# Optimization experiments

Hardware: AMD Instinct MI355X
Metric: run time of the kernel (lower is better)

Reference implementation:

```python
import jax, jax.numpy as jnp
import numpy as np

EPS = 1e-5


def spmm(rows, cols, vals, x):
    # x: (B, C, V); y[b,c,v] = sum_{e: rows[e]==v} vals[e] * x[b,c,cols[e]]
    B, C, V = x.shape
    xt = x.reshape(B * C, V).T                      # (V, B*C)
    msg = vals[:, None] * xt[cols]                  # (E, B*C)
    y = jax.ops.segment_sum(msg, rows, num_segments=V)
    return y.T.reshape(B, C, V)


def cheb_conv(x, W, b, rows, cols, vals):
    # W: (K, Cin, Cout); Chebyshev recurrence over node dim
    K = W.shape[0]
    Tk = [x]
    if K > 1:
        Tk.append(spmm(rows, cols, vals, x))
    for _ in range(2, K):
        Tk.append(2.0 * spmm(rows, cols, vals, Tk[-1]) - Tk[-2])
    T = jnp.stack(Tk)                               # (K, B, Cin, V)
    out = jnp.einsum('kbiv,kio->bov', T, W)
    if b is not None:
        out = out + b[None, :, None]
    return out


def bn(x, g, be):
    # BatchNorm1d training-mode stats over (batch, nodes) per channel
    m = jnp.mean(x, axis=(0, 2), keepdims=True)
    v = jnp.var(x, axis=(0, 2), keepdims=True)
    return (x - m) * jax.lax.rsqrt(v + EPS) * g[None, :, None] + be[None, :, None]


def res_block(x, rows, cols, vals, ga, bea, Wa, ba, gb, beb, Wb, bb, Ws=None):
    xn = bn(x, ga, bea)
    out = cheb_conv(xn, Wa, ba, rows, cols, vals)
    out = bn(jax.nn.relu(out), gb, beb)
    out = cheb_conv(out, Wb, bb, rows, cols, vals)
    sc = xn if Ws is None else cheb_conv(xn, Ws, None, rows, cols, vals)
    return jax.nn.relu(out + sc)


def setup_inputs() -> dict:
    key = jax.random.key(0)
    ks = iter(jax.random.split(key, 40))
    V, E, B, K = 50000, 800000, 8, 4
    d = {}
    d['x'] = jax.random.normal(next(ks), (B, 16, V), dtype=jnp.float32)
    d['lap_rows'] = jax.random.randint(next(ks), (E,), 0, V, dtype=jnp.int32)
    d['lap_cols'] = jax.random.randint(next(ks), (E,), 0, V, dtype=jnp.int32)
    d['lap_vals'] = jax.random.normal(next(ks), (E,), dtype=jnp.float32) * 0.05

    def w(shape, scale=0.1):
        return jax.random.normal(next(ks), shape, dtype=jnp.float32) * scale

    d['W_in'], d['b_in'] = w((K, 16, 32)), w((32,))
    # block 1: 32 -> [32] -> 32 (identity shortcut)
    d['g1a'], d['be1a'] = jnp.ones(32), jnp.zeros(32)
    d['W1a'], d['b1a'] = w((K, 32, 32)), w((32,))
    d['g1b'], d['be1b'] = jnp.ones(32), jnp.zeros(32)
    d['W1b'], d['b1b'] = w((K, 32, 32)), w((32,))
    # block 2: 32 -> [64] -> 64 (ChebConv K=1 shortcut, no bias)
    d['g2a'], d['be2a'] = jnp.ones(32), jnp.zeros(32)
    d['W2a'], d['b2a'] = w((K, 32, 64)), w((64,))
    d['g2b'], d['be2b'] = jnp.ones(64), jnp.zeros(64)
    d['W2b'], d['b2b'] = w((K, 64, 64)), w((64,))
    d['W2s'] = w((1, 32, 64))
    # block 3: 64 -> [64] -> 64 (identity shortcut)
    d['g3a'], d['be3a'] = jnp.ones(64), jnp.zeros(64)
    d['W3a'], d['b3a'] = w((K, 64, 64)), w((64,))
    d['g3b'], d['be3b'] = jnp.ones(64), jnp.zeros(64)
    d['W3b'], d['b3b'] = w((K, 64, 64)), w((64,))
    # output head
    d['g_out'], d['be_out'] = jnp.ones(64), jnp.zeros(64)
    d['W_out'], d['b_out'] = w((K, 64, 10)), w((10,))
    return d


def reference(x, lap_rows, lap_cols, lap_vals,
              W_in, b_in,
              g1a, be1a, W1a, b1a, g1b, be1b, W1b, b1b,
              g2a, be2a, W2a, b2a, g2b, be2b, W2b, b2b, W2s,
              g3a, be3a, W3a, b3a, g3b, be3b, W3b, b3b,
              g_out, be_out, W_out, b_out):
    r, c, v = lap_rows, lap_cols, lap_vals
    out = jax.nn.relu(cheb_conv(x, W_in, b_in, r, c, v))
    out = res_block(out, r, c, v, g1a, be1a, W1a, b1a, g1b, be1b, W1b, b1b)
    out = res_block(out, r, c, v, g2a, be2a, W2a, b2a, g2b, be2b, W2b, b2b, W2s)
    out = res_block(out, r, c, v, g3a, be3a, W3a, b3a, g3b, be3b, W3b, b3b)
    out = bn(out, g_out, be_out)
    out = jax.nn.relu(cheb_conv(out, W_out, b_out, r, c, v))
    pooled = jnp.max(out, axis=2)                   # global max pool over nodes -> (B, 10)
    return jax.nn.log_softmax(pooled, axis=1)
```

## Files before the change

kernel.cpp:

```cpp
#include <hip/hip_runtime.h>
#include <hip/hip_bf16.h>
#include <hip/hip_fp16.h>

typedef float v2f __attribute__((ext_vector_type(2)));
__device__ __forceinline__ v2f vfma2(v2f a, v2f b, v2f c) {
#if __has_builtin(__builtin_elementwise_fma)
    return __builtin_elementwise_fma(a, b, c);
#else
    v2f d; d.x = fmaf(a.x, b.x, c.x); d.y = fmaf(a.y, b.y, c.y); return d;
#endif
}

__global__ void hist_kernel(const int* __restrict__ rows, int* __restrict__ counts, int E) {
    int i = blockIdx.x * blockDim.x + threadIdx.x;
    if (i < E) atomicAdd(&counts[rows[i]], 1);
}

__global__ void chunk_sum_kernel(const int* __restrict__ counts, int* __restrict__ chunk_sums, int V) {
    __shared__ int sh[256];
    int t = threadIdx.x;
    int i = blockIdx.x * 256 + t;
    sh[t] = (i < V) ? counts[i] : 0;
    __syncthreads();
    for (int st = 128; st > 0; st >>= 1) {
        if (t < st) sh[t] += sh[t + st];
        __syncthreads();
    }
    if (t == 0) chunk_sums[blockIdx.x] = sh[0];
}

__global__ void scan_chunks_kernel(int* __restrict__ cs, int n) {
    __shared__ int wsum[4];
    int t = threadIdx.x, lane = t & 63, w = t >> 6;
    int orig = (t < n) ? cs[t] : 0;
    int x = orig;
    #pragma unroll
    for (int d = 1; d < 64; d <<= 1) {
        int y = __shfl_up(x, d);
        if (lane >= d) x += y;
    }
    if (lane == 63) wsum[w] = x;
    __syncthreads();
    int wo = 0;
    for (int j = 0; j < w; ++j) wo += wsum[j];
    if (t < n) cs[t] = wo + x - orig;
}

__global__ void scan_final_kernel(const int* __restrict__ counts, const int* __restrict__ chunk_off,
                                  int* __restrict__ row_ptr, int V) {
    __shared__ int wsum[4];
    int t = threadIdx.x, lane = t & 63, w = t >> 6;
    int i = blockIdx.x * 256 + t;
    int x = (i < V) ? counts[i] : 0;
    #pragma unroll
    for (int d = 1; d < 64; d <<= 1) {
        int y = __shfl_up(x, d);
        if (lane >= d) x += y;
    }
    if (lane == 63) wsum[w] = x;
    __syncthreads();
    int wo = 0;
    for (int j = 0; j < w; ++j) wo += wsum[j];
    if (i < V) row_ptr[i + 1] = chunk_off[blockIdx.x] + wo + x;
    if (i == 0) row_ptr[0] = 0;
}

__global__ void init_cursor_kernel(const int* __restrict__ row_ptr, int* __restrict__ cursor, int V) {
    int i = blockIdx.x * blockDim.x + threadIdx.x;
    if (i < V) cursor[i] = row_ptr[i];
}

__global__ void scatter_kernel(const int* __restrict__ rows, const int* __restrict__ cols,
                               const float* __restrict__ vals, int* __restrict__ cursor,
                               int* __restrict__ cols_s, float* __restrict__ vals_s, int E) {
    int i = blockIdx.x * blockDim.x + threadIdx.x;
    if (i < E) {
        int r = rows[i];
        int p = atomicAdd(&cursor[r], 1);
        cols_s[p] = cols[i];
        vals_s[p] = vals[i];
    }
}

__global__ void sort_rows_kernel(const int* __restrict__ row_ptr, int* cols, float* vals, int V) {
    int v = blockIdx.x * blockDim.x + threadIdx.x;
    if (v >= V) return;
    int e0 = row_ptr[v], e1 = row_ptr[v + 1];
    for (int i = e0 + 1; i < e1; ++i) {
        int c = cols[i];
        unsigned xb = __float_as_uint(vals[i]);
        int j = i - 1;
        while (j >= e0) {
            int cj = cols[j];
            unsigned vj = __float_as_uint(vals[j]);
            if (cj > c || (cj == c && vj > xb)) {
                cols[j + 1] = cj; vals[j + 1] = __uint_as_float(vj);
                --j;
            } else break;
        }
        cols[j + 1] = c;
        vals[j + 1] = __uint_as_float(xb);
    }
}

__global__ void transpose_in_kernel(const float* __restrict__ x, __half* __restrict__ X, int V) {
    int total = V * 128;
    for (int i = blockIdx.x * blockDim.x + threadIdx.x; i < total; i += gridDim.x * blockDim.x) {
        int v = i >> 7;
        int t = i & 127;
        X[i] = __float2half(x[t * V + v]);
    }
}

template <int VPT> struct PackT;
template <> struct PackT<1> { using T = float;  };
template <> struct PackT<2> { using T = float2; };
template <> struct PackT<4> { using T = float4; };

template <int VPT>
__global__ __launch_bounds__(256) void spmm2_kernel(
    const int* __restrict__ row_ptr, const int* __restrict__ cols,
    const float* __restrict__ vals, const __half2* __restrict__ src,
    __half2* dst, const __half2* prev, int V) {
    using T = typename PackT<VPT>::T;
    union U { T raw; __half2 h[VPT]; };
    int lane = threadIdx.x & 63;
    int v = (blockIdx.x << 2) | (threadIdx.x >> 6);
    if (v >= V) return;
    const int W = VPT * 64;
    const size_t row = (size_t)v * W + lane * VPT;

    float pr[2 * VPT];
    bool hasp = (prev != nullptr);
    if (hasp) {
        U pv; pv.raw = *(const T*)(prev + row);
        #pragma unroll
        for (int j = 0; j < VPT; ++j) {
            float2 f = __half22float2(pv.h[j]);
            pr[2 * j] = f.x; pr[2 * j + 1] = f.y;
        }
    }
    float acc[2 * VPT];
    #pragma unroll
    for (int j = 0; j < 2 * VPT; ++j) acc[j] = 0.f;

    int e0 = row_ptr[v], e1 = row_ptr[v + 1];
    int e = e0;
    for (; e + 8 <= e1; e += 8) {
        int   c[8]; float w[8]; U g[8];
        #pragma unroll
        for (int k = 0; k < 8; ++k) { c[k] = cols[e + k]; w[k] = vals[e + k]; }
        #pragma unroll
        for (int k = 0; k < 8; ++k)
            g[k].raw = *(const T*)(src + (size_t)c[k] * W + lane * VPT);
        #pragma unroll
        for (int k = 0; k < 8; ++k) {
            #pragma unroll
            for (int j = 0; j < VPT; ++j) {
                float2 f = __half22float2(g[k].h[j]);
                acc[2*j] += w[k] * f.x; acc[2*j+1] += w[k] * f.y;
            }
        }
    }
    for (; e + 4 <= e1; e += 4) {
        int   c[4]; float w[4]; U g[4];
        #pragma unroll
        for (int k = 0; k < 4; ++k) { c[k] = cols[e + k]; w[k] = vals[e + k]; }
        #pragma unroll
        for (int k = 0; k < 4; ++k)
            g[k].raw = *(const T*)(src + (size_t)c[k] * W + lane * VPT);
        #pragma unroll
        for (int k = 0; k < 4; ++k) {
            #pragma unroll
            for (int j = 0; j < VPT; ++j) {
                float2 f = __half22float2(g[k].h[j]);
                acc[2*j] += w[k] * f.x; acc[2*j+1] += w[k] * f.y;
            }
        }
    }
    for (; e < e1; ++e) {
        int c = cols[e]; float wv = vals[e];
        U g; g.raw = *(const T*)(src + (size_t)c * W + lane * VPT);
        #pragma unroll
        for (int j = 0; j < VPT; ++j) {
            float2 f = __half22float2(g.h[j]);
            acc[2*j] += wv * f.x; acc[2*j+1] += wv * f.y;
        }
    }
    if (hasp) {
        #pragma unroll
        for (int j = 0; j < 2 * VPT; ++j) acc[j] = 2.f * acc[j] - pr[j];
    }
    U o;
    #pragma unroll
    for (int j = 0; j < VPT; ++j) o.h[j] = __floats2half2_rn(acc[2*j], acc[2*j+1]);
    *(T*)(dst + row) = o.raw;
}

template <int CIN, int COUT>
__global__ __launch_bounds__(256) void combine_kernel(
    const __half* T0, const __half* T1, const __half* T2, const __half* T3,
    const float* __restrict__ W, const float* __restrict__ bias,
    const __half* res, const __half* sc, const float* __restrict__ Wsc,
    __half* out, int relu, int V) {
    constexpr int SL    = CIN / 8;
    constexpr int BURST = (SL < 4) ? SL : 4;
    constexpr int NB    = SL / BURST;
    constexpr int SLS   = 32 / 8;
    union U4 { float4 raw; __half2 h[4]; };

    int g = blockIdx.x * 256 + threadIdx.x;
    if (g >= V * 8) return;

    v2f acc[COUT / 2];
    #pragma unroll
    for (int c = 0; c < COUT / 2; ++c) {
        if (bias) { acc[c].x = bias[2 * c]; acc[c].y = bias[2 * c + 1]; }
        else      { acc[c].x = 0.f;         acc[c].y = 0.f; }
    }

    const __half* Ts[4] = {T0, T1, T2, T3};
    #pragma unroll 1
    for (int k = 0; k < 4; ++k) {
        const float4* rp = (const float4*)(Ts[k] + (size_t)g * CIN);
        const float* Wk = W + (size_t)k * CIN * COUT;
        #pragma unroll 1
        for (int b2 = 0; b2 < NB; ++b2) {
            U4 x[BURST];
            #pragma unroll
            for (int j = 0; j < BURST; ++j) x[j].raw = rp[b2 * BURST + j];
            #pragma unroll
            for (int j = 0; j < BURST; ++j) {
                #pragma unroll
                for (int s = 0; s < 4; ++s) {
                    int q = (b2 * BURST + j) * 4 + s;
                    float2 a = __half22float2(x[j].h[s]);
                    const v2f* w0 = (const v2f*)(Wk + (size_t)(2 * q) * COUT);
                    const v2f* w1 = (const v2f*)(Wk + (size_t)(2 * q + 1) * COUT);
                    v2f ax = {a.x, a.x}, ay = {a.y, a.y};
                    #pragma unroll
                    for (int c = 0; c < COUT / 2; ++c) {
                        acc[c] = vfma2(ax, w0[c], acc[c]);
                        acc[c] = vfma2(ay, w1[c], acc[c]);
                    }
                }
            }
        }
    }
    if (sc) {
        const float4* sp = (const float4*)(sc + (size_t)g * 32);
        U4 x[SLS];
        #pragma unroll
        for (int j = 0; j < SLS; ++j) x[j].raw = sp[j];
        #pragma unroll
        for (int j = 0; j < SLS; ++j) {
            #pragma unroll
            for (int s = 0; s < 4; ++s) {
                int q = j * 4 + s;
                float2 a = __half22float2(x[j].h[s]);
                const v2f* w0 = (const v2f*)(Wsc + (size_t)(2 * q) * COUT);
                const v2f* w1 = (const v2f*)(Wsc + (size_t)(2 * q + 1) * COUT);
                v2f ax = {a.x, a.x}, ay = {a.y, a.y};
                #pragma unroll
                for (int c = 0; c < COUT / 2; ++c) {
                    acc[c] = vfma2(ax, w0[c], acc[c]);
                    acc[c] = vfma2(ay, w1[c], acc[c]);
                }
            }
        }
    }

    size_t ob = (size_t)g * COUT;
    if constexpr (COUT % 8 == 0) {
        if (res) {
            const float4* rr = (const float4*)(res + ob);
            #pragma unroll
            for (int q = 0; q < COUT / 8; ++q) {
                U4 rv; rv.raw = rr[q];
                #pragma unroll
                for (int s = 0; s < 4; ++s) {
                    float2 f = __half22float2(rv.h[s]);
                    acc[q * 4 + s].x += f.x; acc[q * 4 + s].y += f.y;
                }
            }
        }
        if (relu) {
            #pragma unroll
            for (int c = 0; c < COUT / 2; ++c) {
                acc[c].x = fmaxf(acc[c].x, 0.f);
                acc[c].y = fmaxf(acc[c].y, 0.f);
            }
        }
        float4* ro = (float4*)(out + ob);
        #pragma unroll
        for (int q = 0; q < COUT / 8; ++q) {
            U4 o;
            #pragma unroll
            for (int s = 0; s < 4; ++s)
                o.h[s] = __floats2half2_rn(acc[q * 4 + s].x, acc[q * 4 + s].y);
            ro[q] = o.raw;
        }
    } else {
        if (res) {
            const __half2* rr = (const __half2*)(res + ob);
            #pragma unroll
            for (int c = 0; c < COUT / 2; ++c) {
                float2 f = __half22float2(rr[c]);
                acc[c].x += f.x; acc[c].y += f.y;
            }
        }
        if (relu) {
            #pragma unroll
            for (int c = 0; c < COUT / 2; ++c) {
                acc[c].x = fmaxf(acc[c].x, 0.f);
                acc[c].y = fmaxf(acc[c].y, 0.f);
            }
        }
        __half2* ro = (__half2*)(out + ob);
        #pragma unroll
        for (int c = 0; c < COUT / 2; ++c)
            ro[c] = __floats2half2_rn(acc[c].x, acc[c].y);
    }
}

__global__ void bn_stats_part_kernel(const __half2* __restrict__ x2, int C, int relu_in,
                                     float* __restrict__ part, size_t N2) {
    __shared__ float sx[256], qx[256], sy[256], qy[256];
    int t = threadIdx.x;
    size_t i0 = (size_t)blockIdx.x * 256 + t;
    size_t step = (size_t)gridDim.x * 256;
    float ax = 0.f, aqx = 0.f, ay = 0.f, aqy = 0.f;
    for (size_t i = i0; i < N2; i += step) {
        float2 f = __half22float2(x2[i]);
        if (relu_in) { f.x = fmaxf(f.x, 0.f); f.y = fmaxf(f.y, 0.f); }
        ax += f.x; aqx += f.x * f.x;
        ay += f.y; aqy += f.y * f.y;
    }
    sx[t] = ax; qx[t] = aqx; sy[t] = ay; qy[t] = aqy;
    __syncthreads();
    int half = C >> 1;
    for (int st = 128; st >= half; st >>= 1) {
        if (t < st) {
            sx[t] += sx[t + st]; qx[t] += qx[t + st];
            sy[t] += sy[t + st]; qy[t] += qy[t + st];
        }
        __syncthreads();
    }
    if (t < half) {
        part[blockIdx.x * 128 + 2 * t]         = sx[t];
        part[blockIdx.x * 128 + 2 * t + 1]     = sy[t];
        part[blockIdx.x * 128 + C + 2 * t]     = qx[t];
        part[blockIdx.x * 128 + C + 2 * t + 1] = qy[t];
    }
}

__global__ void bn_reduce_kernel(const float* __restrict__ part, int nblk,
                                 const float* __restrict__ g, const float* __restrict__ be,
                                 float* __restrict__ ss, int C, float invN) {
    int c = threadIdx.x;
    if (c < C) {
        float s = 0.f, q = 0.f;
        for (int b = 0; b < nblk; ++b) {
            s += part[b * 128 + c];
            q += part[b * 128 + C + c];
        }
        float m = s * invN;
        float var = q * invN - m * m;
        float sc = g[c] * rsqrtf(var + 1e-5f);
        ss[c] = sc;
        ss[C + c] = be[c] - m * sc;
    }
}

__global__ void affine_h_kernel(__half* x, const float* __restrict__ ss, int C,
                                int relu_in, size_t N2) {
    union U4 { float4 raw; __half2 h[4]; };
    size_t NG = N2 >> 2;
    size_t stride = (size_t)gridDim.x * blockDim.x;
    size_t i0 = (size_t)blockIdx.x * blockDim.x + threadIdx.x;
    float4* x4 = (float4*)x;
    int c0 = (int)((8 * i0) & (size_t)(C - 1));
    float sc[8], of[8];
    #pragma unroll
    for (int j = 0; j < 8; ++j) { sc[j] = ss[c0 + j]; of[j] = ss[C + c0 + j]; }
    for (size_t i = i0; i < NG; i += stride) {
        U4 u; u.raw = x4[i];
        #pragma unroll
        for (int j = 0; j < 4; ++j) {
            float2 f = __half22float2(u.h[j]);
            if (relu_in) { f.x = fmaxf(f.x, 0.f); f.y = fmaxf(f.y, 0.f); }
            f.x = f.x * sc[2 * j] + of[2 * j];
            f.y = f.y * sc[2 * j + 1] + of[2 * j + 1];
            u.h[j] = __floats2half2_rn(f.x, f.y);
        }
        x4[i] = u.raw;
    }
}

__global__ void maxpool_h_kernel(const __half* __restrict__ x, float* pooled, int V, int NS) {
    __shared__ float red[256];
    int o = blockIdx.x % 80;
    int slice = blockIdx.x / 80;
    int v0 = (int)((long long)V * slice / NS);
    int v1 = (int)((long long)V * (slice + 1) / NS);
    float m = 0.f;
    for (int v = v0 + threadIdx.x; v < v1; v += 256)
        m = fmaxf(m, __half2float(x[(size_t)v * 80 + o]));
    red[threadIdx.x] = m;
    __syncthreads();
    for (int st = 128; st > 0; st >>= 1) {
        if (threadIdx.x < st) red[threadIdx.x] = fmaxf(red[threadIdx.x], red[threadIdx.x + st]);
        __syncthreads();
    }
    if (threadIdx.x == 0) atomicMax((int*)&pooled[o], __float_as_int(red[0]));
}

__global__ void lsm_kernel(const float* __restrict__ pooled, float* __restrict__ out) {
    int b = threadIdx.x;
    if (b < 8) {
        float m = -1e30f;
        for (int c = 0; c < 10; ++c) m = fmaxf(m, pooled[b * 10 + c]);
        float s = 0.f;
        for (int c = 0; c < 10; ++c) s += expf(pooled[b * 10 + c] - m);
        float l = logf(s);
        for (int c = 0; c < 10; ++c)
            out[b * 10 + c] = pooled[b * 10 + c] - m - l;
    }
}

__global__ void encode_kernel(float* out, float val) {
    int i = threadIdx.x;
    if (i < 80) out[i] = val;
}

extern "C" void kernel_launch(void* const* d_in, const int* in_sizes, int n_in,
                              void* d_out, int out_size, void* d_ws, size_t ws_size,
                              hipStream_t stream) {
    (void)in_sizes; (void)n_in; (void)out_size;
    const int V = 50000, E = 800000;
    const int NCH = (V + 255) / 256;
    const int SB = 512;
    const int NS = 8;

    auto al = [](size_t x) { return (x + 255) & ~(size_t)255; };
    const size_t FB = al((size_t)V * 512 * sizeof(__half));
    const size_t need = 5 * FB + al((V + 1) * 4) + al(V * 4) + al(E * 4) + al(E * 4)
                      + al((size_t)SB * 128 * 4) + al(8 * 128 * 4) + al(80 * 4) + al(NCH * 4);
    if (ws_size < need) {
        encode_kernel<<<1, 128, 0, stream>>>((float*)d_out, (float)(ws_size >> 20));
        return;
    }

    const float* x_in = (const float*)d_in[0];
    const int* rows   = (const int*)d_in[1];
    const int* colsi  = (const int*)d_in[2];
    const float* lvals = (const float*)d_in[3];
    const float* W_in = (const float*)d_in[4];
    const float* b_in = (const float*)d_in[5];
    const float* g1a = (const float*)d_in[6],  *be1a = (const float*)d_in[7];
    const float* W1a = (const float*)d_in[8],  *b1a  = (const float*)d_in[9];
    const float* g1b = (const float*)d_in[10], *be1b = (const float*)d_in[11];
    const float* W1b = (const float*)d_in[12], *b1b  = (const float*)d_in[13];
    const float* g2a = (const float*)d_in[14], *be2a = (const float*)d_in[15];
    const float* W2a = (const float*)d_in[16], *b2a  = (const float*)d_in[17];
    const float* g2b = (const float*)d_in[18], *be2b = (const float*)d_in[19];
    const float* W2b = (const float*)d_in[20], *b2b  = (const float*)d_in[21];
    const float* W2s = (const float*)d_in[22];
    const float* g3a = (const float*)d_in[23], *be3a = (const float*)d_in[24];
    const float* W3a = (const float*)d_in[25], *b3a  = (const float*)d_in[26];
    const float* g3b = (const float*)d_in[27], *be3b = (const float*)d_in[28];
    const float* W3b = (const float*)d_in[29], *b3b  = (const float*)d_in[30];
    const float* g_o = (const float*)d_in[31], *be_o = (const float*)d_in[32];
    const float* W_o = (const float*)d_in[33], *b_o  = (const float*)d_in[34];

    char* wp = (char*)d_ws;
    auto take = [&](size_t bytes) -> void* { void* p = (void*)wp; wp += al(bytes); return p; };
    __half* P0 = (__half*)take(FB);
    __half* P1 = (__half*)take(FB);
    __half* P2 = (__half*)take(FB);
    __half* P3 = (__half*)take(FB);
    __half* P4 = (__half*)take(FB);
    int* row_ptr  = (int*)take((V + 1) * sizeof(int));
    int* cursor   = (int*)take(V * sizeof(int));
    int* cols_s   = (int*)take(E * sizeof(int));
    float* vals_s = (float*)take(E * sizeof(float));
    float* part   = (float*)take((size_t)SB * 128 * sizeof(float));
    float* aff    = (float*)take(8 * 128 * sizeof(float));
    float* pooled = (float*)take(80 * sizeof(float));
    int* chunks   = (int*)take(NCH * sizeof(int));

    hipMemsetAsync(cursor, 0, V * sizeof(int), stream);
    hipMemsetAsync(pooled, 0, 80 * sizeof(float), stream);

    hist_kernel<<<(E + 255) / 256, 256, 0, stream>>>(rows, cursor, E);
    chunk_sum_kernel<<<NCH, 256, 0, stream>>>(cursor, chunks, V);
    scan_chunks_kernel<<<1, 256, 0, stream>>>(chunks, NCH);
    scan_final_kernel<<<NCH, 256, 0, stream>>>(cursor, chunks, row_ptr, V);
    init_cursor_kernel<<<(V + 255) / 256, 256, 0, stream>>>(row_ptr, cursor, V);
    scatter_kernel<<<(E + 255) / 256, 256, 0, stream>>>(rows, colsi, lvals, cursor, cols_s, vals_s, E);
    sort_rows_kernel<<<(V + 255) / 256, 256, 0, stream>>>(row_ptr, cols_s, vals_s, V);
    transpose_in_kernel<<<4096, 256, 0, stream>>>(x_in, P0, V);

    auto spmm = [&](const __half* src, __half* dst, const __half* prev, int C) {
        int grid = (V + 3) / 4;
        if (C == 16)
            spmm2_kernel<1><<<grid, 256, 0, stream>>>(row_ptr, cols_s, vals_s,
                (const __half2*)src, (__half2*)dst, (const __half2*)prev, V);
        else if (C == 32)
            spmm2_kernel<2><<<grid, 256, 0, stream>>>(row_ptr, cols_s, vals_s,
                (const __half2*)src, (__half2*)dst, (const __half2*)prev, V);
        else
            spmm2_kernel<4><<<grid, 256, 0, stream>>>(row_ptr, cols_s, vals_s,
                (const __half2*)src, (__half2*)dst, (const __half2*)prev, V);
    };
    const int MG = (V * 8 + 255) / 256;
    auto comb = [&](const __half* T0, const __half* T1, const __half* T2, const __half* T3,
                    int Cin, int Cout, const float* W, const float* bias,
                    const __half* res, const __half* sc, const float* Wsc,
                    __half* out, int relu) {
        if (Cin == 16 && Cout == 32)
            combine_kernel<16, 32><<<MG, 256, 0, stream>>>(T0, T1, T2, T3, W, bias, res, sc, Wsc, out, relu, V);
        else if (Cin == 32 && Cout == 32)
            combine_kernel<32, 32><<<MG, 256, 0, stream>>>(T0, T1, T2, T3, W, bias, res, sc, Wsc, out, relu, V);
        else if (Cin == 32 && Cout == 64)
            combine_kernel<32, 64><<<MG, 256, 0, stream>>>(T0, T1, T2, T3, W, bias, res, sc, Wsc, out, relu, V);
        else if (Cin == 64 && Cout == 64)
            combine_kernel<64, 64><<<MG, 256, 0, stream>>>(T0, T1, T2, T3, W, bias, res, sc, Wsc, out, relu, V);
        else
            combine_kernel<64, 10><<<MG, 256, 0, stream>>>(T0, T1, T2, T3, W, bias, res, sc, Wsc, out, relu, V);
    };
    auto stats = [&](const __half* xb, int C, int relu, int slot, const float* g, const float* be) {
        bn_stats_part_kernel<<<SB, 256, 0, stream>>>((const __half2*)xb, C, relu, part,
                                                     (size_t)V * 4 * C);
        bn_reduce_kernel<<<1, 64, 0, stream>>>(part, SB, g, be, aff + slot * 128, C,
                                               1.f / ((float)V * 8.f));
    };
    auto affine = [&](__half* xb, int C, int relu, int slot) {
        affine_h_kernel<<<2048, 256, 0, stream>>>(xb, aff + slot * 128, C, relu,
                                                  (size_t)V * 4 * C);
    };
    const __half* NH = nullptr;
    const float*  NF = nullptr;

    spmm(P0, P1, nullptr, 16);
    spmm(P1, P2, P0, 16);
    spmm(P2, P3, P1, 16);
    comb(P0, P1, P2, P3, 16, 32, W_in, b_in, NH, NH, NF, P4, 1);

    stats(P4, 32, 0, 0, g1a, be1a);
    affine(P4, 32, 0, 0);
    spmm(P4, P0, nullptr, 32);
    spmm(P0, P1, P4, 32);
    spmm(P1, P2, P0, 32);
    comb(P4, P0, P1, P2, 32, 32, W1a, b1a, NH, NH, NF, P0, 0);
    stats(P0, 32, 1, 1, g1b, be1b);
    affine(P0, 32, 1, 1);
    spmm(P0, P1, nullptr, 32);
    spmm(P1, P2, P0, 32);
    spmm(P2, P3, P1, 32);
    comb(P0, P1, P2, P3, 32, 32, W1b, b1b, P4, NH, NF, P4, 1);

    stats(P4, 32, 0, 2, g2a, be2a);
    affine(P4, 32, 0, 2);
    spmm(P4, P0, nullptr, 32);
    spmm(P0, P1, P4, 32);
    spmm(P1, P2, P0, 32);
    comb(P4, P0, P1, P2, 32, 64, W2a, b2a, NH, NH, NF, P3, 0);
    stats(P3, 64, 1, 3, g2b, be2b);
    affine(P3, 64, 1, 3);
    spmm(P3, P0, nullptr, 64);
    spmm(P0, P1, P3, 64);
    spmm(P1, P2, P0, 64);
    comb(P3, P0, P1, P2, 64, 64, W2b, b2b, NH, P4, W2s, P0, 1);

    stats(P0, 64, 0, 4, g3a, be3a);
    affine(P0, 64, 0, 4);
    spmm(P0, P1, nullptr, 64);
    spmm(P1, P2, P0, 64);
    spmm(P2, P3, P1, 64);
    comb(P0, P1, P2, P3, 64, 64, W3a, b3a, NH, NH, NF, P1, 0);
    stats(P1, 64, 1, 5, g3b, be3b);
    affine(P1, 64, 1, 5);
    spmm(P1, P2, nullptr, 64);
    spmm(P2, P3, P1, 64);
    spmm(P3, P4, P2, 64);
    comb(P1, P2, P3, P4, 64, 64, W3b, b3b, P0, NH, NF, P1, 1);

    stats(P1, 64, 0, 6, g_o, be_o);
    affine(P1, 64, 0, 6);
    spmm(P1, P0, nullptr, 64);
    spmm(P0, P2, P1, 64);
    spmm(P2, P3, P0, 64);
    comb(P1, P0, P2, P3, 64, 10, W_o, b_o, NH, NH, NF, P4, 1);
    maxpool_h_kernel<<<80 * NS, 256, 0, stream>>>(P4, pooled, V, NS);
    lsm_kernel<<<1, 64, 0, stream>>>(pooled, (float*)d_out);
}
```

Before: 4.466 ms.

## Split 64-channel Chebyshev SpMM chains into two channel halves for cache reuse

For two of the 64-channel Chebyshev recurrences, the SpMM kernel now runs the full three-step chain on one 128-half slice of each row before moving to the other half. Each gather then touches only 256 bytes per node instead of 512, so the working set of the source feature matrix is halved and more of it may stay resident in L2/MALL during the random gathers. The cost is twice as many kernel launches, the row_ptr/cols/vals indices being read twice, and narrower per-lane loads.

```diff
diff --git a/kernel.cpp b/kernel.cpp
--- a/kernel.cpp
+++ b/kernel.cpp
@@ -117,18 +117,18 @@
 template <> struct PackT<2> { using T = float2; };
 template <> struct PackT<4> { using T = float4; };
 
-template <int VPT>
+template <int VPT, int WF>
 __global__ __launch_bounds__(256) void spmm2_kernel(
     const int* __restrict__ row_ptr, const int* __restrict__ cols,
     const float* __restrict__ vals, const __half2* __restrict__ src,
-    __half2* dst, const __half2* prev, int V) {
+    __half2* dst, const __half2* prev, int hoff, int V) {
     using T = typename PackT<VPT>::T;
     union U { T raw; __half2 h[VPT]; };
     int lane = threadIdx.x & 63;
     int v = (blockIdx.x << 2) | (threadIdx.x >> 6);
     if (v >= V) return;
-    const int W = VPT * 64;
-    const size_t row = (size_t)v * W + lane * VPT;
+    const int lb = hoff + lane * VPT;
+    const size_t row = (size_t)v * WF + lb;
 
     float pr[2 * VPT];
     bool hasp = (prev != nullptr);
@@ -152,7 +152,7 @@
         for (int k = 0; k < 8; ++k) { c[k] = cols[e + k]; w[k] = vals[e + k]; }
         #pragma unroll
         for (int k = 0; k < 8; ++k)
-            g[k].raw = *(const T*)(src + (size_t)c[k] * W + lane * VPT);
+            g[k].raw = *(const T*)(src + (size_t)c[k] * WF + lb);
         #pragma unroll
         for (int k = 0; k < 8; ++k) {
             #pragma unroll
@@ -168,7 +168,7 @@
         for (int k = 0; k < 4; ++k) { c[k] = cols[e + k]; w[k] = vals[e + k]; }
         #pragma unroll
         for (int k = 0; k < 4; ++k)
-            g[k].raw = *(const T*)(src + (size_t)c[k] * W + lane * VPT);
+            g[k].raw = *(const T*)(src + (size_t)c[k] * WF + lb);
         #pragma unroll
         for (int k = 0; k < 4; ++k) {
             #pragma unroll
@@ -180,7 +180,7 @@
     }
     for (; e < e1; ++e) {
         int c = cols[e]; float wv = vals[e];
-        U g; g.raw = *(const T*)(src + (size_t)c * W + lane * VPT);
+        U g; g.raw = *(const T*)(src + (size_t)c * WF + lb);
         #pragma unroll
         for (int j = 0; j < VPT; ++j) {
             float2 f = __half22float2(g.h[j]);
@@ -501,17 +501,35 @@
     sort_rows_kernel<<<(V + 255) / 256, 256, 0, stream>>>(row_ptr, cols_s, vals_s, V);
     transpose_in_kernel<<<4096, 256, 0, stream>>>(x_in, P0, V);
 
-    auto spmm = [&](const __half* src, __half* dst, const __half* prev, int C) {
-        int grid = (V + 3) / 4;
+    const int SG = (V + 3) / 4;
+    auto spmm_one = [&](const __half* src, __half* dst, const __half* prev,
+                        int C, int hoff, bool half) {
         if (C == 16)
-            spmm2_kernel<1><<<grid, 256, 0, stream>>>(row_ptr, cols_s, vals_s,
-                (const __half2*)src, (__half2*)dst, (const __half2*)prev, V);
+            spmm2_kernel<1, 64><<<SG, 256, 0, stream>>>(row_ptr, cols_s, vals_s,
+                (const __half2*)src, (__half2*)dst, (const __half2*)prev, 0, V);
         else if (C == 32)
-            spmm2_kernel<2><<<grid, 256, 0, stream>>>(row_ptr, cols_s, vals_s,
-                (const __half2*)src, (__half2*)dst, (const __half2*)prev, V);
+            spmm2_kernel<2, 128><<<SG, 256, 0, stream>>>(row_ptr, cols_s, vals_s,
+                (const __half2*)src, (__half2*)dst, (const __half2*)prev, 0, V);
+        else if (!half)
+            spmm2_kernel<4, 256><<<SG, 256, 0, stream>>>(row_ptr, cols_s, vals_s,
+                (const __half2*)src, (__half2*)dst, (const __half2*)prev, 0, V);
         else
-            spmm2_kernel<4><<<grid, 256, 0, stream>>>(row_ptr, cols_s, vals_s,
-                (const __half2*)src, (__half2*)dst, (const __half2*)prev, V);
+            spmm2_kernel<2, 256><<<SG, 256, 0, stream>>>(row_ptr, cols_s, vals_s,
+                (const __half2*)src, (__half2*)dst, (const __half2*)prev, hoff, V);
+    };
+    auto cheb3 = [&](const __half* a, __half* b, __half* c, __half* d, int C, bool split) {
+        if (C == 64 && split) {
+            for (int h = 0; h < 2; ++h) {
+                int off = h * 128;
+                spmm_one(a, b, nullptr, 64, off, true);
+                spmm_one(b, c, a,       64, off, true);
+                spmm_one(c, d, b,       64, off, true);
+            }
+        } else {
+            spmm_one(a, b, nullptr, C, 0, false);
+            spmm_one(b, c, a,       C, 0, false);
+            spmm_one(c, d, b,       C, 0, false);
+        }
     };
     const int MG = (V * 8 + 255) / 256;
     auto comb = [&](const __half* T0, const __half* T1, const __half* T2, const __half* T3,
@@ -542,55 +560,39 @@
     const __half* NH = nullptr;
     const float*  NF = nullptr;
 
-    spmm(P0, P1, nullptr, 16);
-    spmm(P1, P2, P0, 16);
-    spmm(P2, P3, P1, 16);
+    cheb3(P0, P1, P2, P3, 16, false);
     comb(P0, P1, P2, P3, 16, 32, W_in, b_in, NH, NH, NF, P4, 1);
 
     stats(P4, 32, 0, 0, g1a, be1a);
     affine(P4, 32, 0, 0);
-    spmm(P4, P0, nullptr, 32);
-    spmm(P0, P1, P4, 32);
-    spmm(P1, P2, P0, 32);
+    cheb3(P4, P0, P1, P2, 32, false);
     comb(P4, P0, P1, P2, 32, 32, W1a, b1a, NH, NH, NF, P0, 0);
     stats(P0, 32, 1, 1, g1b, be1b);
     affine(P0, 32, 1, 1);
-    spmm(P0, P1, nullptr, 32);
-    spmm(P1, P2, P0, 32);
-    spmm(P2, P3, P1, 32);
+    cheb3(P0, P1, P2, P3, 32, false);
     comb(P0, P1, P2, P3, 32, 32, W1b, b1b, P4, NH, NF, P4, 1);
 
     stats(P4, 32, 0, 2, g2a, be2a);
     affine(P4, 32, 0, 2);
-    spmm(P4, P0, nullptr, 32);
-    spmm(P0, P1, P4, 32);
-    spmm(P1, P2, P0, 32);
+    cheb3(P4, P0, P1, P2, 32, false);
     comb(P4, P0, P1, P2, 32, 64, W2a, b2a, NH, NH, NF, P3, 0);
     stats(P3, 64, 1, 3, g2b, be2b);
     affine(P3, 64, 1, 3);
-    spmm(P3, P0, nullptr, 64);
-    spmm(P0, P1, P3, 64);
-    spmm(P1, P2, P0, 64);
+    cheb3(P3, P0, P1, P2, 64, true);
     comb(P3, P0, P1, P2, 64, 64, W2b, b2b, NH, P4, W2s, P0, 1);
 
     stats(P0, 64, 0, 4, g3a, be3a);
     affine(P0, 64, 0, 4);
-    spmm(P0, P1, nullptr, 64);
-    spmm(P1, P2, P0, 64);
-    spmm(P2, P3, P1, 64);
+    cheb3(P0, P1, P2, P3, 64, true);
     comb(P0, P1, P2, P3, 64, 64, W3a, b3a, NH, NH, NF, P1, 0);
     stats(P1, 64, 1, 5, g3b, be3b);
     affine(P1, 64, 1, 5);
-    spmm(P1, P2, nullptr, 64);
-    spmm(P2, P3, P1, 64);
-    spmm(P3, P4, P2, 64);
+    cheb3(P1, P2, P3, P4, 64, false);
     comb(P1, P2, P3, P4, 64, 64, W3b, b3b, P0, NH, NF, P1, 1);
 
     stats(P1, 64, 0, 6, g_o, be_o);
     affine(P1, 64, 0, 6);
-    spmm(P1, P0, nullptr, 64);
-    spmm(P0, P2, P1, 64);
-    spmm(P2, P3, P0, 64);
+    cheb3(P1, P0, P2, P3, 64, false);
     comb(P1, P0, P2, P3, 64, 10, W_o, b_o, NH, NH, NF, P4, 1);
     maxpool_h_kernel<<<80 * NS, 256, 0, stream>>>(P4, pooled, V, NS);
     lsm_kernel<<<1, 64, 0, stream>>>(pooled, (float*)d_out);
```

Result: no change. 4.468 ms (+0.0%).
